# Optimization experiments

Hardware: AMD Instinct MI355X
Metric: run time of the kernel (lower is better)

Reference implementation:

```python
import jax, jax.numpy as jnp
import numpy as np

WS = 7            # window_size
HEADS = 12
HEAD_DIM = 32
DIM = 384
INNER = HEADS * HEAD_DIM
DISP = WS // 2    # displacement for shifted windows


def _rel_indices():
    idx = np.array([[x, y] for x in range(WS) for y in range(WS)])  # (49,2)
    d = idx[None, :, :] - idx[:, None, :] + WS - 1                   # (49,49,2), values in [0, 2*WS-2]
    return d


def _masks():
    # upper/lower mask (applied to last row of windows)
    ul = np.zeros((WS * WS, WS * WS), np.float32)
    ul[-DISP * WS:, :-DISP * WS] = -np.inf
    ul[:-DISP * WS, -DISP * WS:] = -np.inf
    # left/right mask (applied to last column of windows)
    lr = np.zeros((WS, WS, WS, WS), np.float32)
    lr[:, -DISP:, :, :-DISP] = -np.inf
    lr[:, :-DISP, :, -DISP:] = -np.inf
    lr = lr.reshape(WS * WS, WS * WS)
    return ul, lr


_RI = _rel_indices()
_UL, _LR = _masks()


def setup_inputs() -> dict:
    key = jax.random.key(0)
    k1, k2, k3, k4, k5 = jax.random.split(key, 5)
    b, H, W = 32, 56, 56
    x = jax.random.normal(k1, (b, H, W, DIM), jnp.float32)
    w_qkv = jax.random.normal(k2, (DIM, 3 * INNER), jnp.float32) * (DIM ** -0.5)
    pos_emb = jax.random.normal(k3, (2 * WS - 1, 2 * WS - 1), jnp.float32)
    w_out = jax.random.normal(k4, (INNER, DIM), jnp.float32) * (INNER ** -0.5)
    b_out = jax.random.normal(k5, (DIM,), jnp.float32)
    return {"x": x, "w_qkv": w_qkv, "pos_emb": pos_emb, "w_out": w_out, "b_out": b_out}


def reference(x, w_qkv, pos_emb, w_out, b_out):
    b, H, W, _ = x.shape
    nwh, nww = H // WS, W // WS
    # cyclic shift
    x = jnp.roll(x, (-DISP, -DISP), (1, 2))
    qkv = x @ w_qkv                                     # [b,H,W,3*INNER]
    q, k, v = jnp.split(qkv, 3, axis=-1)

    def to_win(t):
        # [b,H,W,INNER] -> [b, heads, n_windows, WS*WS, head_dim]
        t = t.reshape(b, nwh, WS, nww, WS, HEADS, HEAD_DIM)
        return t.transpose(0, 5, 1, 3, 2, 4, 6).reshape(b, HEADS, nwh * nww, WS * WS, HEAD_DIM)

    q, k, v = map(to_win, (q, k, v))
    dots = jnp.einsum('bhwid,bhwjd->bhwij', q, k) * (HEAD_DIM ** -0.5)
    # relative position bias gather
    dots = dots + pos_emb[_RI[:, :, 0], _RI[:, :, 1]]
    # shifted-window masks: last row of windows and last column of windows
    dots = dots.at[:, :, -nww:].add(jnp.asarray(_UL))
    dots = dots.at[:, :, nww - 1::nww].add(jnp.asarray(_LR))
    attn = jax.nn.softmax(dots, axis=-1)
    out = jnp.einsum('bhwij,bhwjd->bhwid', attn, v)
    # windows back to image layout
    out = out.reshape(b, HEADS, nwh, nww, WS, WS, HEAD_DIM)
    out = out.transpose(0, 2, 4, 3, 5, 1, 6).reshape(b, H, W, INNER)
    out = out @ w_out + b_out
    return jnp.roll(out, (DISP, DISP), (1, 2))
```

## Files before the change

### kernel.cpp

```cpp
#include <hip/hip_runtime.h>

typedef __attribute__((ext_vector_type(8))) short short8;
typedef __attribute__((ext_vector_type(4))) short short4v;
typedef __attribute__((ext_vector_type(4))) float f32x4;
typedef __attribute__((ext_vector_type(2))) int int2v;

#define MFMA(a, b, c) __builtin_amdgcn_mfma_f32_16x16x32_bf16(a, b, c, 0, 0, 0)
#define SCALE 0.17677669529663687f

__device__ __forceinline__ short f2bf(float f) {
  union { float f; unsigned u; } v;
  v.f = f;
  unsigned r = v.u + 0x7fffu + ((v.u >> 16) & 1u);
  return (short)(r >> 16);
}

__device__ __forceinline__ unsigned cvt_pk(float lo, float hi) {
  unsigned r;
  asm("v_cvt_pk_bf16_f32 %0, %1, %2" : "=v"(r) : "v"(lo), "v"(hi));
  return r;
}

#define XS_STR 392
#define QK_STR 264
#define P_STR  72
#define AO_STR 392

__global__ void prep_weights(const float* __restrict__ wqkv,
                             const float* __restrict__ wout,
                             short* __restrict__ wqkvT,
                             short* __restrict__ woutT) {
  int i = blockIdx.x * 256 + threadIdx.x;
  if (i < 1152 * 384) {
    int n = i / 384, k = i - (i / 384) * 384;
    float w = wqkv[k * 1152 + n];
    if (n < 384) w *= SCALE;
    wqkvT[i] = f2bf(w);
  }
  if (i < 384 * 384) {
    int n = i / 384, k = i - (i / 384) * 384;
    woutT[i] = f2bf(wout[k * 384 + n]);
  }
}

__global__ void prep_bias(const float* __restrict__ pe, float* __restrict__ btabT) {
  int id = blockIdx.x * 256 + threadIdx.x;
  if (id >= 16384) return;
  int t = id >> 12;
  int i = (id >> 6) & 63;
  int j = id & 63;
  float v;
  if (i < 49 && j < 49) {
    int ai = i / 7, bi = i - ai * 7, aj = j / 7, bj = j - aj * 7;
    v = pe[(aj - ai + 6) * 13 + (bj - bi + 6)];
    if ((t & 1) && ((i >= 28) != (j >= 28))) v = -1e30f;
    if ((t & 2) && ((bi >= 4) != (bj >= 4))) v = -1e30f;
  } else if (j < 49) {
    v = 0.f;
  } else {
    v = -1e30f;
  }
  btabT[((t * 64 + i) * 16 + (j & 15)) * 4 + (j >> 4)] = v;
}

#define GEMM_STEP(BUF)                                                        \
  {                                                                           \
    short8 a0 = *(const short8*)(pA[0] + k * 32);                             \
    short8 a1 = *(const short8*)(pA[1] + k * 32);                             \
    short8 a2 = *(const short8*)(pA[2] + k * 32);                             \
    short8 a3 = *(const short8*)(pA[3] + k * 32);                             \
    acc[0][0] = MFMA(a0, BUF[0], acc[0][0]);                                  \
    acc[1][0] = MFMA(a1, BUF[0], acc[1][0]);                                  \
    acc[2][0] = MFMA(a2, BUF[0], acc[2][0]);                                  \
    acc[3][0] = MFMA(a3, BUF[0], acc[3][0]);                                  \
    acc[0][1] = MFMA(a0, BUF[1], acc[0][1]);                                  \
    acc[1][1] = MFMA(a1, BUF[1], acc[1][1]);                                  \
    acc[2][1] = MFMA(a2, BUF[1], acc[2][1]);                                  \
    acc[3][1] = MFMA(a3, BUF[1], acc[3][1]);                                  \
    acc[0][2] = MFMA(a0, BUF[2], acc[0][2]);                                  \
    acc[1][2] = MFMA(a1, BUF[2], acc[1][2]);                                  \
    acc[2][2] = MFMA(a2, BUF[2], acc[2][2]);                                  \
    acc[3][2] = MFMA(a3, BUF[2], acc[3][2]);                                  \
  }

#define GEMM_PIPELINE()                                                       \
  _Pragma("unroll")                                                           \
  for (int n = 0; n < 3; ++n) bA[n] = *(const short8*)(pB[n]);                \
  _Pragma("unroll")                                                           \
  for (int n = 0; n < 3; ++n) bB[n] = *(const short8*)(pB[n] + 32);           \
  _Pragma("unroll")                                                           \
  for (int k = 0; k < 12; ++k) {                                              \
    if (k + 2 < 12) {                                                         \
      const int off = (k + 2) * 32;                                           \
      if (k % 3 == 0) {                                                       \
        _Pragma("unroll")                                                     \
        for (int n = 0; n < 3; ++n) bC[n] = *(const short8*)(pB[n] + off);    \
      } else if (k % 3 == 1) {                                                \
        _Pragma("unroll")                                                     \
        for (int n = 0; n < 3; ++n) bA[n] = *(const short8*)(pB[n] + off);    \
      } else {                                                                \
        _Pragma("unroll")                                                     \
        for (int n = 0; n < 3; ++n) bB[n] = *(const short8*)(pB[n] + off);    \
      }                                                                       \
    }                                                                         \
    if (k % 3 == 0) GEMM_STEP(bA)                                             \
    else if (k % 3 == 1) GEMM_STEP(bB)                                        \
    else GEMM_STEP(bC)                                                        \
  }

__global__ __launch_bounds__(512, 4) void swin_qkv_attn(
    const float* __restrict__ x, const short* __restrict__ wqkvT,
    const float* __restrict__ btabT, short* __restrict__ aout) {

  __shared__ short xs[49 * XS_STR];
  __shared__ short qk[49 * QK_STR];
  __shared__ short vT[128 * 64];

  const int tid = threadIdx.x;
  const int lane = tid & 63;
  const int wv = tid >> 6;
  const int l15 = lane & 15;
  const int lhi = lane >> 4;

  const int bid = blockIdx.x;
  const int sw = (bid & 7) * 768 + (bid >> 3);
  const int g = sw - (sw / 3) * 3;
  const int bw = sw / 3;
  const int batch = bw >> 6;
  const int win = bw & 63;
  const int wy = win >> 3, wx = win & 7;

  const size_t xbase = (size_t)batch * (56 * 56 * 384);
  const f32x4 zf = {0.f, 0.f, 0.f, 0.f};

  {
    int* vz = (int*)vT;
    for (int t2 = tid; t2 < 4096; t2 += 512) vz[t2] = 0;
  }

  for (int t = tid; t < 49 * 96; t += 512) {
    int tok = t / 96;
    int seg = t - tok * 96;
    int iy = (tok * 37) >> 8;
    int ix = tok - iy * 7;
    int r = wy * 7 + iy + 3; if (r >= 56) r -= 56;
    int c = wx * 7 + ix + 3; if (c >= 56) c -= 56;
    const float4 v = *(const float4*)(x + xbase + (size_t)(r * 56 + c) * 384 + seg * 4);
    int2v o;
    o.x = (int)cvt_pk(v.x, v.y);
    o.y = (int)cvt_pk(v.z, v.w);
    *(int2v*)(&xs[tok * XS_STR + seg * 4]) = o;
  }
  __syncthreads();

  {
    const int n0 = wv * 48;
    const short* pB[3];
#pragma unroll
    for (int n = 0; n < 3; ++n) {
      const int c0 = n0 + n * 16;
      const int seg = c0 >> 7;
      const int hloc = (c0 >> 5) & 3;
      const int wrow = seg * 384 + (g * 4 + hloc) * 32 + (c0 & 31);
      pB[n] = wqkvT + (size_t)(wrow + l15) * 384 + lhi * 8;
    }
    f32x4 acc[4][3];
#pragma unroll
    for (int m = 0; m < 4; ++m)
#pragma unroll
      for (int n = 0; n < 3; ++n) acc[m][n] = zf;

    const short* pA[4];
#pragma unroll
    for (int m = 0; m < 4; ++m) {
      int row = m * 16 + l15;
      int rc = row < 49 ? row : 48;
      pA[m] = &xs[rc * XS_STR + lhi * 8];
    }

    short8 bA[3], bB[3], bC[3];
    GEMM_PIPELINE()

#pragma unroll
    for (int n = 0; n < 3; ++n) {
      const int c0 = n0 + n * 16;
#pragma unroll
      for (int m = 0; m < 4; ++m)
#pragma unroll
        for (int r = 0; r < 4; ++r) {
          int row = m * 16 + lhi * 4 + r;
          if (row < 49) {
            if (c0 < 256) {
              qk[row * QK_STR + c0 + l15] = f2bf(acc[m][n][r]);
            } else {
              const int d = c0 - 256 + l15;
              *(short*)((char*)vT + d * 128 + ((2 * row) ^ ((d & 7) << 4))) =
                  f2bf(acc[m][n][r]);
            }
          }
        }
    }
  }
  __syncthreads();

  {
    const int hl = wv >> 1;
    const int mh = wv & 1;
    const int tt = (wy == 7 ? 1 : 0) | (wx == 7 ? 2 : 0);
    short* Pbuf = &xs[wv * 2304];

    f32x4 bb[2][4];
#pragma unroll
    for (int mi = 0; mi < 2; ++mi)
#pragma unroll
      for (int r = 0; r < 4; ++r) {
        const int i = mh * 32 + mi * 16 + lhi * 4 + r;
        bb[mi][r] = *(const f32x4*)(&btabT[((tt * 64 + i) * 16 + l15) * 4]);
      }

    short8 qa[2];
#pragma unroll
    for (int mi = 0; mi < 2; ++mi) {
      int row = mh * 32 + mi * 16 + l15;
      int rc = row < 49 ? row : 48;
      qa[mi] = *(const short8*)(&qk[rc * QK_STR + hl * 32 + lhi * 8]);
    }
    f32x4 s[2][4];
#pragma unroll
    for (int nt = 0; nt < 4; ++nt) {
      int jr = nt * 16 + l15;
      int jc = jr < 49 ? jr : 48;
      short8 kb = *(const short8*)(&qk[jc * QK_STR + 128 + hl * 32 + lhi * 8]);
#pragma unroll
      for (int mi = 0; mi < 2; ++mi) s[mi][nt] = MFMA(qa[mi], kb, zf);
    }

#pragma unroll
    for (int mi = 0; mi < 2; ++mi)
#pragma unroll
      for (int r = 0; r < 4; ++r)
#pragma unroll
        for (int nt = 0; nt < 4; ++nt)
          s[mi][nt][r] += bb[mi][r][nt];

#pragma unroll
    for (int mi = 0; mi < 2; ++mi)
#pragma unroll
      for (int r = 0; r < 4; ++r) {
        float mx = fmaxf(fmaxf(s[mi][0][r], s[mi][1][r]),
                         fmaxf(s[mi][2][r], s[mi][3][r]));
        mx = fmaxf(mx, __shfl_xor(mx, 1));
        mx = fmaxf(mx, __shfl_xor(mx, 2));
        mx = fmaxf(mx, __shfl_xor(mx, 4));
        mx = fmaxf(mx, __shfl_xor(mx, 8));
        float p0 = __expf(s[mi][0][r] - mx);
        float p1 = __expf(s[mi][1][r] - mx);
        float p2 = __expf(s[mi][2][r] - mx);
        float p3 = __expf(s[mi][3][r] - mx);
        float sum = p0 + p1 + p2 + p3;
        sum += __shfl_xor(sum, 1);
        sum += __shfl_xor(sum, 2);
        sum += __shfl_xor(sum, 4);
        sum += __shfl_xor(sum, 8);
        const float inv = __builtin_amdgcn_rcpf(sum);
        const int rowl = mi * 16 + lhi * 4 + r;
        Pbuf[rowl * P_STR +  0 + l15] = f2bf(p0 * inv);
        Pbuf[rowl * P_STR + 16 + l15] = f2bf(p1 * inv);
        Pbuf[rowl * P_STR + 32 + l15] = f2bf(p2 * inv);
        Pbuf[rowl * P_STR + 48 + l15] = f2bf(p3 * inv);
      }

    f32x4 O[2][2];
#pragma unroll
    for (int mi = 0; mi < 2; ++mi)
#pragma unroll
      for (int n2 = 0; n2 < 2; ++n2) O[mi][n2] = zf;

#pragma unroll
    for (int ks = 0; ks < 2; ++ks) {
      short8 pa[2];
#pragma unroll
      for (int mi = 0; mi < 2; ++mi)
        pa[mi] = *(const short8*)(&Pbuf[(mi * 16 + l15) * P_STR + ks * 32 + lhi * 8]);
#pragma unroll
      for (int n2 = 0; n2 < 2; ++n2) {
        const int dg = hl * 32 + n2 * 16 + l15;
        const short8 vb = *(const short8*)((const char*)vT + dg * 128 +
                              ((ks * 64 + lhi * 16) ^ ((dg & 7) << 4)));
#pragma unroll
        for (int mi = 0; mi < 2; ++mi) O[mi][n2] = MFMA(pa[mi], vb, O[mi][n2]);
      }
    }

    short* ab = aout + (size_t)bw * (49 * 384) + (g * 4 + hl) * 32;
#pragma unroll
    for (int mi = 0; mi < 2; ++mi)
#pragma unroll
      for (int n2 = 0; n2 < 2; ++n2)
#pragma unroll
        for (int r = 0; r < 4; ++r) {
          int row = mh * 32 + mi * 16 + lhi * 4 + r;
          if (row < 49) ab[row * 384 + n2 * 16 + l15] = f2bf(O[mi][n2][r]);
        }
  }
}

__global__ __launch_bounds__(512, 4) void swin_outproj(
    const short* __restrict__ aout, const short* __restrict__ woutT,
    const float* __restrict__ bout, float* __restrict__ out) {

  __shared__ short ao[49 * AO_STR];

  const int tid = threadIdx.x;
  const int lane = tid & 63;
  const int wv = tid >> 6;
  const int l15 = lane & 15;
  const int lhi = lane >> 4;

  const int bw = blockIdx.x;
  const int batch = bw >> 6;
  const int win = bw & 63;
  const int wy = win >> 3, wx = win & 7;

  const size_t xbase = (size_t)batch * (56 * 56 * 384);
  const f32x4 zf = {0.f, 0.f, 0.f, 0.f};

  const short* abg = aout + (size_t)bw * (49 * 384);
  for (int t = tid; t < 49 * 48; t += 512) {
    int row = t / 48;
    int seg = t - row * 48;
    *(short8*)(&ao[row * AO_STR + seg * 8]) = *(const short8*)(&abg[row * 384 + seg * 8]);
  }
  __syncthreads();

  {
    const int n0 = wv * 48;
    f32x4 acc[4][3];
#pragma unroll
    for (int m = 0; m < 4; ++m)
#pragma unroll
      for (int n = 0; n < 3; ++n) acc[m][n] = zf;

    const short* pB[3];
#pragma unroll
    for (int n = 0; n < 3; ++n)
      pB[n] = woutT + (size_t)(n0 + n * 16 + l15) * 384 + lhi * 8;

    const short* pA[4];
#pragma unroll
    for (int m = 0; m < 4; ++m) {
      int row = m * 16 + l15;
      int rc = row < 49 ? row : 48;
      pA[m] = &ao[rc * AO_STR + lhi * 8];
    }

    short8 bA[3], bB[3], bC[3];
    GEMM_PIPELINE()

    float bo[3];
#pragma unroll
    for (int n = 0; n < 3; ++n) bo[n] = bout[n0 + n * 16 + l15];

#pragma unroll
    for (int m = 0; m < 4; ++m)
#pragma unroll
      for (int r = 0; r < 4; ++r) {
        const int row = m * 16 + lhi * 4 + r;
        if (row < 49) {
          int iy = (row * 37) >> 8, ix = row - iy * 7;
          int rr = wy * 7 + iy + 3; if (rr >= 56) rr -= 56;
          int cc = wx * 7 + ix + 3; if (cc >= 56) cc -= 56;
          float* dst = out + xbase + (size_t)(rr * 56 + cc) * 384 + n0;
#pragma unroll
          for (int n = 0; n < 3; ++n) dst[n * 16 + l15] = acc[m][n][r] + bo[n];
        }
      }
  }
}

extern "C" void kernel_launch(void* const* d_in, const int* in_sizes, int n_in,
                              void* d_out, int out_size, void* d_ws, size_t ws_size,
                              hipStream_t stream) {
  const float* x    = (const float*)d_in[0];
  const float* wqkv = (const float*)d_in[1];
  const float* pos  = (const float*)d_in[2];
  const float* wout = (const float*)d_in[3];
  const float* bo   = (const float*)d_in[4];

  char* ws = (char*)d_ws;
  short* wqkvT = (short*)ws;                         ws += 1152 * 384 * 2;
  short* woutT = (short*)ws;                         ws += 384 * 384 * 2;
  float* btabT = (float*)ws;                         ws += 4 * 64 * 16 * 4 * 4;
  short* aoutg = (short*)ws;

  prep_weights<<<1728, 256, 0, stream>>>(wqkv, wout, wqkvT, woutT);
  prep_bias<<<64, 256, 0, stream>>>(pos, btabT);
  swin_qkv_attn<<<6144, 512, 0, stream>>>(x, wqkvT, btabT, aoutg);
  swin_outproj<<<2048, 512, 0, stream>>>(aoutg, woutT, bo, (float*)d_out);
}
```

Baseline: 401.6 us.

## Alias QKV attention shared memory into one buffer to raise occupancy

Folds the separate x-tile, Q/K and transposed-V shared buffers into a single LDS region. After the QKV GEMM finishes reading x, Q, K and V are written over it, and the softmax P tiles are then staged in the Q area. Q and K get an XOR-swizzled layout, the V zero-fill is dropped because all 64 rows are now written, and launch bounds rise to 6 blocks to allow more resident blocks per CU. The price is extra block-wide barriers, and more register pressure from holding the accumulators, probabilities and V fragments across those barriers.

Result: slower. 548.5 us (+36.6%).

```diff
diff --git a/kernel.cpp b/kernel.cpp
--- a/kernel.cpp
+++ b/kernel.cpp
@@ -1,7 +1,6 @@
 #include <hip/hip_runtime.h>
 
 typedef __attribute__((ext_vector_type(8))) short short8;
-typedef __attribute__((ext_vector_type(4))) short short4v;
 typedef __attribute__((ext_vector_type(4))) float f32x4;
 typedef __attribute__((ext_vector_type(2))) int int2v;
 
@@ -21,10 +20,12 @@
   return r;
 }
 
-#define XS_STR 392
-#define QK_STR 264
+#define XS_STR 424
 #define P_STR  72
 #define AO_STR 392
+#define VT_OFF 0
+#define Q_OFF  16384
+#define K_OFF  28928
 
 __global__ void prep_weights(const float* __restrict__ wqkv,
                              const float* __restrict__ wout,
@@ -108,13 +109,12 @@
     else GEMM_STEP(bC)                                                        \
   }
 
-__global__ __launch_bounds__(512, 4) void swin_qkv_attn(
+__global__ __launch_bounds__(512, 6) void swin_qkv_attn(
     const float* __restrict__ x, const short* __restrict__ wqkvT,
     const float* __restrict__ btabT, short* __restrict__ aout) {
 
-  __shared__ short xs[49 * XS_STR];
-  __shared__ short qk[49 * QK_STR];
-  __shared__ short vT[128 * 64];
+  __shared__ short smemA[49 * XS_STR];
+  char* smc = (char*)smemA;
 
   const int tid = threadIdx.x;
   const int lane = tid & 63;
@@ -132,11 +132,6 @@
 
   const size_t xbase = (size_t)batch * (56 * 56 * 384);
   const f32x4 zf = {0.f, 0.f, 0.f, 0.f};
-
-  {
-    int* vz = (int*)vT;
-    for (int t2 = tid; t2 < 4096; t2 += 512) vz[t2] = 0;
-  }
 
   for (int t = tid; t < 49 * 96; t += 512) {
     int tok = t / 96;
@@ -149,12 +144,13 @@
     int2v o;
     o.x = (int)cvt_pk(v.x, v.y);
     o.y = (int)cvt_pk(v.z, v.w);
-    *(int2v*)(&xs[tok * XS_STR + seg * 4]) = o;
+    *(int2v*)(&smemA[tok * XS_STR + seg * 4]) = o;
   }
   __syncthreads();
 
+  f32x4 acc[4][3];
+  const int n0 = wv * 48;
   {
-    const int n0 = wv * 48;
     const short* pB[3];
 #pragma unroll
     for (int n = 0; n < 3; ++n) {
@@ -164,7 +160,6 @@
       const int wrow = seg * 384 + (g * 4 + hloc) * 32 + (c0 & 31);
       pB[n] = wqkvT + (size_t)(wrow + l15) * 384 + lhi * 8;
     }
-    f32x4 acc[4][3];
 #pragma unroll
     for (int m = 0; m < 4; ++m)
 #pragma unroll
@@ -175,12 +170,15 @@
     for (int m = 0; m < 4; ++m) {
       int row = m * 16 + l15;
       int rc = row < 49 ? row : 48;
-      pA[m] = &xs[rc * XS_STR + lhi * 8];
+      pA[m] = &smemA[rc * XS_STR + lhi * 8];
     }
 
     short8 bA[3], bB[3], bC[3];
     GEMM_PIPELINE()
-
+  }
+  __syncthreads();
+
+  {
 #pragma unroll
     for (int n = 0; n < 3; ++n) {
       const int c0 = n0 + n * 16;
@@ -188,15 +186,19 @@
       for (int m = 0; m < 4; ++m)
 #pragma unroll
         for (int r = 0; r < 4; ++r) {
-          int row = m * 16 + lhi * 4 + r;
-          if (row < 49) {
-            if (c0 < 256) {
-              qk[row * QK_STR + c0 + l15] = f2bf(acc[m][n][r]);
-            } else {
-              const int d = c0 - 256 + l15;
-              *(short*)((char*)vT + d * 128 + ((2 * row) ^ ((d & 7) << 4))) =
+          const int row = m * 16 + lhi * 4 + r;
+          if (c0 < 256) {
+            if (row < 49) {
+              const int f = c0 + l15;
+              const int base = (f < 128) ? Q_OFF : K_OFF;
+              const int fo = (f & 127) * 2;
+              *(short*)(smc + base + row * 256 + (fo ^ ((row & 7) << 4))) =
                   f2bf(acc[m][n][r]);
             }
+          } else {
+            const int d = c0 - 256 + l15;
+            *(short*)(smc + VT_OFF + d * 128 + ((2 * row) ^ ((d & 7) << 4))) =
+                f2bf(acc[m][n][r]);
           }
         }
     }
@@ -207,7 +209,6 @@
     const int hl = wv >> 1;
     const int mh = wv & 1;
     const int tt = (wy == 7 ? 1 : 0) | (wx == 7 ? 2 : 0);
-    short* Pbuf = &xs[wv * 2304];
 
     f32x4 bb[2][4];
 #pragma unroll
@@ -223,14 +224,16 @@
     for (int mi = 0; mi < 2; ++mi) {
       int row = mh * 32 + mi * 16 + l15;
       int rc = row < 49 ? row : 48;
-      qa[mi] = *(const short8*)(&qk[rc * QK_STR + hl * 32 + lhi * 8]);
+      qa[mi] = *(const short8*)(smc + Q_OFF + rc * 256 +
+                                ((hl * 64 + lhi * 16) ^ ((rc & 7) << 4)));
     }
     f32x4 s[2][4];
 #pragma unroll
     for (int nt = 0; nt < 4; ++nt) {
       int jr = nt * 16 + l15;
       int jc = jr < 49 ? jr : 48;
-      short8 kb = *(const short8*)(&qk[jc * QK_STR + 128 + hl * 32 + lhi * 8]);
+      short8 kb = *(const short8*)(smc + K_OFF + jc * 256 +
+                                   ((hl * 64 + lhi * 16) ^ ((jc & 7) << 4)));
 #pragma unroll
       for (int mi = 0; mi < 2; ++mi) s[mi][nt] = MFMA(qa[mi], kb, zf);
     }
@@ -263,33 +266,43 @@
         sum += __shfl_xor(sum, 4);
         sum += __shfl_xor(sum, 8);
         const float inv = __builtin_amdgcn_rcpf(sum);
-        const int rowl = mi * 16 + lhi * 4 + r;
-        Pbuf[rowl * P_STR +  0 + l15] = f2bf(p0 * inv);
-        Pbuf[rowl * P_STR + 16 + l15] = f2bf(p1 * inv);
-        Pbuf[rowl * P_STR + 32 + l15] = f2bf(p2 * inv);
-        Pbuf[rowl * P_STR + 48 + l15] = f2bf(p3 * inv);
+        s[mi][0][r] = p0 * inv;
+        s[mi][1][r] = p1 * inv;
+        s[mi][2][r] = p2 * inv;
+        s[mi][3][r] = p3 * inv;
       }
 
-    f32x4 O[2][2];
-#pragma unroll
-    for (int mi = 0; mi < 2; ++mi)
-#pragma unroll
-      for (int n2 = 0; n2 < 2; ++n2) O[mi][n2] = zf;
-
-#pragma unroll
-    for (int ks = 0; ks < 2; ++ks) {
-      short8 pa[2];
-#pragma unroll
-      for (int mi = 0; mi < 2; ++mi)
-        pa[mi] = *(const short8*)(&Pbuf[(mi * 16 + l15) * P_STR + ks * 32 + lhi * 8]);
+    short8 vb[2][2];
+#pragma unroll
+    for (int ks = 0; ks < 2; ++ks)
 #pragma unroll
       for (int n2 = 0; n2 < 2; ++n2) {
         const int dg = hl * 32 + n2 * 16 + l15;
-        const short8 vb = *(const short8*)((const char*)vT + dg * 128 +
-                              ((ks * 64 + lhi * 16) ^ ((dg & 7) << 4)));
-#pragma unroll
-        for (int mi = 0; mi < 2; ++mi) O[mi][n2] = MFMA(pa[mi], vb, O[mi][n2]);
+        vb[ks][n2] = *(const short8*)(smc + VT_OFF + dg * 128 +
+                                      ((ks * 64 + lhi * 16) ^ ((dg & 7) << 4)));
       }
+
+    __syncthreads();
+
+    char* Pb = smc + Q_OFF + wv * 2304;
+    f32x4 O[2][2];
+#pragma unroll
+    for (int mi = 0; mi < 2; ++mi) {
+#pragma unroll
+      for (int r = 0; r < 4; ++r) {
+        const int rowl = lhi * 4 + r;
+        short* pr = (short*)(Pb + rowl * 144);
+        pr[ 0 + l15] = f2bf(s[mi][0][r]);
+        pr[16 + l15] = f2bf(s[mi][1][r]);
+        pr[32 + l15] = f2bf(s[mi][2][r]);
+        pr[48 + l15] = f2bf(s[mi][3][r]);
+      }
+      const short8 pa0 = *(const short8*)(Pb + l15 * 144 +  0 + lhi * 16);
+      const short8 pa1 = *(const short8*)(Pb + l15 * 144 + 64 + lhi * 16);
+      O[mi][0] = MFMA(pa0, vb[0][0], zf);
+      O[mi][1] = MFMA(pa0, vb[0][1], zf);
+      O[mi][0] = MFMA(pa1, vb[1][0], O[mi][0]);
+      O[mi][1] = MFMA(pa1, vb[1][1], O[mi][1]);
     }
 
     short* ab = aout + (size_t)bw * (49 * 384) + (g * 4 + hl) * 32;
```
